# Optimization experiments

Measured on AMD Instinct MI355X. Metric: run time of the kernel, lower is better.

## Reference

```python
import jax, jax.numpy as jnp
import numpy as np

N, E = 50000, 800000
NUM_TYPES = 5
NUM_HEADS = 4
HIDDEN = 32
IN_DIM = 128
NEG_SLOPE = 0.2


def typed_linear(x, types, W):
    # x: [M, in], types: [M] int, W: [T, in, out] -> [M, out]
    out = jnp.zeros((x.shape[0], W.shape[2]), dtype=x.dtype)
    for t in range(W.shape[0]):
        out = out + jnp.where((types == t)[:, None], x @ W[t], jnp.zeros((), x.dtype))
    return out


def setup_inputs() -> dict:
    key = jax.random.key(0)
    ks = jax.random.split(key, 10)
    x = jax.random.normal(ks[0], (N, IN_DIM), dtype=jnp.float32)
    ntype = jax.random.randint(ks[1], (N,), 0, NUM_TYPES)
    etype = jax.random.randint(ks[2], (E,), 0, NUM_TYPES)
    src = jax.random.randint(ks[3], (E,), 0, N)
    dst = jax.random.randint(ks[4], (E,), 0, N)
    sc = 1.0 / np.sqrt(IN_DIM)
    W_typed = jax.random.normal(ks[5], (NUM_TYPES, IN_DIM, HIDDEN * NUM_HEADS), dtype=jnp.float32) * sc
    al_w = jax.random.normal(ks[6], (NUM_TYPES, HIDDEN, HIDDEN), dtype=jnp.float32) * (1.0 / np.sqrt(HIDDEN))
    ar_w = jax.random.normal(ks[7], (NUM_TYPES, HIDDEN, HIDDEN), dtype=jnp.float32) * (1.0 / np.sqrt(HIDDEN))
    W_res = jax.random.normal(ks[8], (IN_DIM, HIDDEN * NUM_HEADS), dtype=jnp.float32) * sc
    b_res = jax.random.normal(ks[9], (HIDDEN * NUM_HEADS,), dtype=jnp.float32) * 0.01
    return {"x": x, "ntype": ntype, "etype": etype, "src": src, "dst": dst,
            "W_typed": W_typed, "al_w": al_w, "ar_w": ar_w, "W_res": W_res, "b_res": b_res}


def reference(x, ntype, etype, src, dst, W_typed, al_w, ar_w, W_res, b_res):
    n = x.shape[0]
    # typed projection W (dropout in the original is applied to `feat` but discarded)
    feat = typed_linear(x, ntype, W_typed)                    # [N, H*D]
    h = feat.reshape(n, NUM_HEADS, HIDDEN)                    # [N, H, D]
    ntype_rep = jnp.repeat(ntype, NUM_HEADS)                  # row n*H+h has node n's type
    h_flat = h.reshape(-1, HIDDEN)
    h_l = typed_linear(h_flat, ntype_rep, al_w).reshape(n, NUM_HEADS, HIDDEN).sum(-1)  # [N, H]
    h_r = typed_linear(h_flat, ntype_rep, ar_w).reshape(n, NUM_HEADS, HIDDEN).sum(-1)  # [N, H]
    e = jax.nn.leaky_relu(h_l[src] + h_r[dst], NEG_SLOPE)     # [E, H]
    # edge softmax grouped by destination node
    m = jax.ops.segment_max(e, dst, num_segments=n)           # [N, H]
    ex = jnp.exp(e - m[dst])
    s = jax.ops.segment_sum(ex, dst, num_segments=n)          # [N, H]
    alpha = ex / s[dst]                                       # [E, H]
    # u_mul_e + sum aggregation
    msg = h[src] * alpha[:, :, None]                          # [E, H, D]
    agg = jax.ops.segment_sum(msg, dst, num_segments=n)       # [N, H, D]
    out = agg.transpose(0, 2, 1).reshape(n, HIDDEN * NUM_HEADS)  # matches permute(0,2,1).view
    out = out + x @ W_res + b_res                             # residual
    return jax.nn.relu(out)                                   # activation
```

## Files before the change

kernel.cpp:

```cpp
#include <hip/hip_runtime.h>
#include <cstdint>
#include <cstddef>

#define IN_DIM 128
#define HID 32
#define NH 4
#define OUT_DIM 128
#define NEG 0.2f
#define NT 5
#define BPT 16
#define NCOLS 272
#define NTILE 17
#define TILE_ELEMS 2048
#define CAPN 50048
#define NE1 144
#define NPREP 40
#define RSHIFT 7
#define SLOT0 16
#define MAXD 56

typedef __attribute__((ext_vector_type(8))) __bf16 bf16x8;
typedef __attribute__((ext_vector_type(4))) float f32x4;

static __device__ __forceinline__ float leaky(float v) { return v > 0.f ? v : NEG * v; }
static __device__ __forceinline__ float blo(unsigned u) { return __uint_as_float(u << 16); }
static __device__ __forceinline__ float bhi(unsigned u) { return __uint_as_float(u & 0xffff0000u); }

static __device__ __forceinline__ void scat1(char* __restrict__ rec, int d, int s) {
    char* rp = rec + ((size_t)d << RSHIFT);
    int r = atomicAdd((int*)rp, 1);
    if (r < MAXD) *(unsigned short*)(rp + SLOT0 + 2 * r) = (unsigned short)s;
}

static __device__ __forceinline__ void scatter4(const int4* __restrict__ dst4,
                                                const int4* __restrict__ src4,
                                                char* __restrict__ rec,
                                                int gid, int E4) {
    if (gid >= E4) return;
    int4 d = dst4[gid];
    int4 s = src4[gid];
    char* rp0 = rec + ((size_t)d.x << RSHIFT);
    char* rp1 = rec + ((size_t)d.y << RSHIFT);
    char* rp2 = rec + ((size_t)d.z << RSHIFT);
    char* rp3 = rec + ((size_t)d.w << RSHIFT);
    int r0 = atomicAdd((int*)rp0, 1);
    int r1 = atomicAdd((int*)rp1, 1);
    int r2 = atomicAdd((int*)rp2, 1);
    int r3 = atomicAdd((int*)rp3, 1);
    if (r0 < MAXD) *(unsigned short*)(rp0 + SLOT0 + 2 * r0) = (unsigned short)s.x;
    if (r1 < MAXD) *(unsigned short*)(rp1 + SLOT0 + 2 * r1) = (unsigned short)s.y;
    if (r2 < MAXD) *(unsigned short*)(rp2 + SLOT0 + 2 * r2) = (unsigned short)s.z;
    if (r3 < MAXD) *(unsigned short*)(rp3 + SLOT0 + 2 * r3) = (unsigned short)s.w;
}

__global__ void __launch_bounds__(256) setup_kernel(
        const int4* __restrict__ dst4, const int4* __restrict__ src4,
        char* __restrict__ rec, int E,
        const int* __restrict__ ntype, int* __restrict__ tcur, int* __restrict__ order,
        int N, int nbs,
        const float* __restrict__ Wt, const float* __restrict__ Wres,
        const float* __restrict__ alw, const float* __restrict__ arw,
        __bf16* __restrict__ Whi, __bf16* __restrict__ Wlo) {
    __shared__ int lc[NT];
    __shared__ int gb[NT];
    __shared__ float alv[HID], arv[HID];
    int bid = blockIdx.x, tid = threadIdx.x;

    if (bid < NE1) {
        int E4 = E >> 2;
        scatter4(dst4, src4, rec, bid * 256 + tid, E4);
        if (bid == 0 && tid == 0) {
            const int* dsts = (const int*)dst4;
            const int* srcs = (const int*)src4;
            for (int e = E4 << 2; e < E; ++e) scat1(rec, dsts[e], srcs[e]);
        }
        return;
    }
    bid -= NE1;
    if (bid < nbs) {
        if (tid < NT) lc[tid] = 0;
        __syncthreads();
        int gid = bid * 256 + tid;
        int t = -1, rank = 0;
        if (gid < N) {
            t = ntype[gid];
            rank = atomicAdd(&lc[t], 1);
        }
        __syncthreads();
        if (tid < NT && lc[tid] > 0) gb[tid] = atomicAdd(&tcur[tid], lc[tid]);
        __syncthreads();
        if (gid < N) order[t * CAPN + gb[t] + rank] = gid;
        return;
    }
    bid -= nbs;
    {
        int t = bid >> 3, part = bid & 7;
        if (tid < 64) {
            int which = tid >= HID;
            int i = tid & (HID - 1);
            const float* p = (which ? arw : alw) + ((size_t)t * HID + i) * HID;
            float s = 0.f;
            for (int j = 0; j < HID; ++j) s += p[j];
            (which ? arv : alv)[i] = s;
        }
        __syncthreads();
        int end = (part + 1) * 4352;
        for (int idx = part * 4352 + tid; idx < end; idx += 256) {
            int n = idx >> 7, k = idx & 127;
            float w;
            if (n < 128) {
                w = Wt[((size_t)t * IN_DIM + k) * OUT_DIM + n];
            } else if (n < 256) {
                w = Wres[(size_t)k * OUT_DIM + (n - 128)];
            } else if (n < 264) {
                int h = (n - 256) & 3;
                const float* av = (n >= 260) ? arv : alv;
                float s = 0.f;
                for (int i = 0; i < HID; ++i)
                    s += Wt[((size_t)t * IN_DIM + k) * OUT_DIM + h * HID + i] * av[i];
                w = s;
            } else {
                w = 0.f;
            }
            __bf16 hi = (__bf16)w;
            __bf16 lo = (__bf16)(w - (float)hi);
            size_t o = (size_t)(t * NTILE + (n >> 4)) * TILE_ELEMS
                     + (size_t)(((k >> 3) * 16 + (n & 15)) << 3) + (k & 7);
            Whi[o] = hi;
            Wlo[o] = lo;
        }
    }
}

__global__ void __launch_bounds__(256) mega2_kernel(
        const int4* __restrict__ dst4, const int4* __restrict__ src4,
        char* __restrict__ rec, int E,
        int e4base, int nbh2,
        const float* __restrict__ x, const int* __restrict__ order,
        const int* __restrict__ tcur,
        const __bf16* __restrict__ Whi, const __bf16* __restrict__ Wlo,
        const float* __restrict__ bres,
        __bf16* __restrict__ h_bf, float* __restrict__ hl, float* __restrict__ hr,
        float* __restrict__ out) {
    __shared__ bf16x8 lds_hi[256];
    __shared__ bf16x8 lds_lo[256];
    __shared__ int nids_s[BPT];
    int bid = blockIdx.x;
    int q = bid / 5, r5 = bid - q * 5;
    int tid = threadIdx.x;

    if (r5 == 4) {
        if (q >= nbh2) return;
        scatter4(dst4, src4, rec, e4base + q * 256 + tid, E >> 2);
        return;
    }

    int b = 4 * q + r5;
    int t = -1, lb = 0, cthis = 0;
    {
        int pbl = 0;
        for (int tt = 0; tt < NT; ++tt) {
            int c = tcur[tt];
            int ntt = (c + BPT - 1) >> 4;
            if (b < pbl + ntt) { t = tt; lb = b - pbl; cthis = c; break; }
            pbl += ntt;
        }
    }
    if (t < 0) return;
    int base = lb * BPT;

    {
        int row = tid >> 4, c = tid & 15;
        int li = base + row;
        int nd = (li < cthis) ? order[t * CAPN + li] : -1;
        if (tid < BPT) nids_s[tid] = (base + tid < cthis) ? order[t * CAPN + base + tid] : -1;
        float4 v0 = make_float4(0.f, 0.f, 0.f, 0.f), v1 = v0;
        if (nd >= 0) {
            const float4* xr = (const float4*)(x + (size_t)nd * IN_DIM + c * 8);
            v0 = xr[0];
            v1 = xr[1];
        }
        float f[8] = {v0.x, v0.y, v0.z, v0.w, v1.x, v1.y, v1.z, v1.w};
        bf16x8 hv, lv;
#pragma unroll
        for (int j = 0; j < 8; ++j) {
            __bf16 h = (__bf16)f[j];
            hv[j] = h;
            lv[j] = (__bf16)(f[j] - (float)h);
        }
        lds_hi[c * 16 + row] = hv;
        lds_lo[c * 16 + row] = lv;
    }
    __syncthreads();

    int w = tid >> 6, lane = tid & 63;
    int lr = lane & 15, lg = lane >> 4;
    bool w3 = (w == 3);

    const __bf16* Wbh = Whi + (size_t)t * NTILE * TILE_ELEMS;
    const __bf16* Wbl = Wlo + (size_t)t * NTILE * TILE_ELEMS;

    f32x4 acc[5];
#pragma unroll
    for (int nt = 0; nt < 5; ++nt) acc[nt] = (f32x4)0.f;

#pragma unroll
    for (int ks = 0; ks < 4; ++ks) {
        int ai = ks * 64 + lg * 16 + lr;
        size_t ao = (size_t)ai << 3;
        bf16x8 ah = lds_hi[ai];
        bf16x8 al = lds_lo[ai];
#pragma unroll
        for (int nt = 0; nt < 5; ++nt) {
            if (nt == 4 && !w3) continue;
            int ng = (nt < 4) ? (nt * 4 + w) : 16;
            bf16x8 bh = *(const bf16x8*)(Wbh + (size_t)ng * TILE_ELEMS + ao);
            acc[nt] = __builtin_amdgcn_mfma_f32_16x16x32_bf16(al, bh, acc[nt], 0, 0, 0);
            acc[nt] = __builtin_amdgcn_mfma_f32_16x16x32_bf16(ah, bh, acc[nt], 0, 0, 0);
            if (nt == 4) {
                bf16x8 bl = *(const bf16x8*)(Wbl + (size_t)16 * TILE_ELEMS + ao);
                acc[4] = __builtin_amdgcn_mfma_f32_16x16x32_bf16(ah, bl, acc[4], 0, 0, 0);
            }
        }
    }

    int nids[4];
#pragma unroll
    for (int r = 0; r < 4; ++r) nids[r] = nids_s[lg * 4 + r];

#pragma unroll
    for (int nt = 0; nt < 5; ++nt) {
        if (nt == 4 && !w3) continue;
        int ng = (nt < 4) ? (nt * 4 + w) : 16;
        int col = ng * 16 + lr;
        float bb = (col >= 128 && col < 256) ? bres[col - 128] : 0.f;
#pragma unroll
        for (int r = 0; r < 4; ++r) {
            int nid = nids[r];
            if (nid < 0) continue;
            float v = acc[nt][r];
            if (col < 128) {
                h_bf[(size_t)nid * OUT_DIM + col] = (__bf16)v;
            } else if (col < 256) {
                out[(size_t)nid * OUT_DIM + (col - 128)] = v + bb;
            } else if (col < 260) {
                hl[nid * NH + (col - 256)] = v;
            } else if (col < 264) {
                hr[nid * NH + (col - 260)] = v;
            }
        }
    }
}

__global__ void agg_kernel(const char* __restrict__ rec,
                           const float* __restrict__ hlf,
                           const float4* __restrict__ hr4, const __bf16* __restrict__ h_bf,
                           float* __restrict__ out, int n_nodes) {
    int gid = blockIdx.x * 256 + threadIdx.x;
    int n = gid >> 4;
    if (n >= n_nodes) return;
    int l = threadIdx.x & 15;
    int myh = l >> 2;
    const char* rp = rec + ((size_t)n << RSHIFT);
    int deg = *(const int*)rp;
    if (deg > MAXD) deg = MAXD;
    const unsigned short* ss = (const unsigned short*)(rp + SLOT0);
    float acc[8];
#pragma unroll
    for (int m = 0; m < 8; ++m) acc[m] = 0.f;

    if (deg > 0) {
        float4 hv = hr4[n];
        float hrh = myh < 2 ? (myh == 0 ? hv.x : hv.y) : (myh == 2 ? hv.z : hv.w);
        float sw = 0.f;
        int k = 0;
        for (; k + 8 <= deg; k += 8) {
            uint4 sp = *(const uint4*)(ss + k);
            int sv[8];
            sv[0] = sp.x & 0xffff; sv[1] = sp.x >> 16;
            sv[2] = sp.y & 0xffff; sv[3] = sp.y >> 16;
            sv[4] = sp.z & 0xffff; sv[5] = sp.z >> 16;
            sv[6] = sp.w & 0xffff; sv[7] = sp.w >> 16;
            uint4 u[8];
            float e[8];
#pragma unroll
            for (int j = 0; j < 8; ++j) {
                u[j] = *(const uint4*)(h_bf + (size_t)sv[j] * OUT_DIM + l * 8);
                e[j] = hlf[sv[j] * 4 + myh];
            }
#pragma unroll
            for (int j = 0; j < 8; ++j) {
                float wv = __expf(leaky(e[j] + hrh));
                sw += wv;
                acc[0] += wv * blo(u[j].x); acc[1] += wv * bhi(u[j].x);
                acc[2] += wv * blo(u[j].y); acc[3] += wv * bhi(u[j].y);
                acc[4] += wv * blo(u[j].z); acc[5] += wv * bhi(u[j].z);
                acc[6] += wv * blo(u[j].w); acc[7] += wv * bhi(u[j].w);
            }
        }
        for (; k < deg; ++k) {
            int sv0 = ss[k];
            uint4 u0 = *(const uint4*)(h_bf + (size_t)sv0 * OUT_DIM + l * 8);
            float e0 = hlf[sv0 * 4 + myh];
            float wv = __expf(leaky(e0 + hrh));
            sw += wv;
            acc[0] += wv * blo(u0.x); acc[1] += wv * bhi(u0.x);
            acc[2] += wv * blo(u0.y); acc[3] += wv * bhi(u0.y);
            acc[4] += wv * blo(u0.z); acc[5] += wv * bhi(u0.z);
            acc[6] += wv * blo(u0.w); acc[7] += wv * bhi(u0.w);
        }
        float inv_s = 1.f / sw;
#pragma unroll
        for (int m = 0; m < 8; ++m) acc[m] *= inv_s;
    }
    size_t ob = (size_t)n * OUT_DIM;
    int based = (l & 3) << 3;
#pragma unroll
    for (int m = 0; m < 8; ++m) {
        int j = ((based + m) << 2) | myh;
        out[ob + j] = fmaxf(acc[m] + out[ob + j], 0.f);
    }
}

extern "C" void kernel_launch(void* const* d_in, const int* in_sizes, int n_in,
                              void* d_out, int out_size, void* d_ws, size_t ws_size,
                              hipStream_t stream) {
    const float* x     = (const float*)d_in[0];
    const int*   ntype = (const int*)d_in[1];
    const int*   src   = (const int*)d_in[3];
    const int*   dst   = (const int*)d_in[4];
    const float* Wt    = (const float*)d_in[5];
    const float* alw   = (const float*)d_in[6];
    const float* arw   = (const float*)d_in[7];
    const float* Wres  = (const float*)d_in[8];
    const float* bres  = (const float*)d_in[9];
    float* out = (float*)d_out;
    int N = in_sizes[1];
    int E = in_sizes[3];

    char* ws = (char*)d_ws;
    size_t off = 0;
    auto alloc = [&](size_t bytes) -> char* {
        char* p = ws + off;
        off += (bytes + 255) & ~(size_t)255;
        return p;
    };
    __bf16* h_bf       = (__bf16*)alloc((size_t)N * OUT_DIM * 2);
    float*  hl         = (float*)alloc((size_t)N * NH * 4);
    float*  hr         = (float*)alloc((size_t)N * NH * 4);
    int*    order      = (int*)alloc((size_t)NT * CAPN * 4);
    __bf16* Whi        = (__bf16*)alloc((size_t)NT * NTILE * TILE_ELEMS * 2);
    __bf16* Wlo        = (__bf16*)alloc((size_t)NT * NTILE * TILE_ELEMS * 2);
    char*   zstart     = ws + off;
    char*   rec        = (char*)alloc((size_t)N << RSHIFT);
    int*    tcur       = (int*)alloc(NT * 4);
    size_t  zlen       = (ws + off) - zstart;

    hipMemsetAsync(zstart, 0, zlen, stream);

    int nbs = (N + 255) / 256;
    int E4 = E >> 2;
    int e4base = NE1 * 256;
    int rem4 = E4 > e4base ? E4 - e4base : 0;
    int nbh2 = (rem4 + 255) / 256;

    setup_kernel<<<NE1 + nbs + NPREP, 256, 0, stream>>>(
        (const int4*)dst, (const int4*)src, rec, E,
        ntype, tcur, order, N, nbs,
        Wt, Wres, alw, arw, Whi, Wlo);

    int pbmax = (N + BPT - 1) / BPT + NT;
    int qproj = (pbmax + 3) / 4;
    int qmax = qproj > nbh2 ? qproj : nbh2;
    mega2_kernel<<<5 * qmax, 256, 0, stream>>>(
        (const int4*)dst, (const int4*)src, rec, E, e4base, nbh2,
        x, order, tcur, Whi, Wlo, bres, h_bf, hl, hr, out);

    agg_kernel<<<(N * 16 + 255) / 256, 256, 0, stream>>>(rec, hl, (const float4*)hr,
                                                         h_bf, out, N);
}
```

Baseline: 117.6 us.

## Replace global atomic edge scatter with two-pass bucketed binning by destination

Edges are first binned into 256-node destination buckets, using a shared-memory histogram and one global atomic per bucket per block. Each bucket is then expanded into per-node adjacency slots inside the projection kernel using only shared-memory atomics. This replaces one global atomic per edge on the padded record array and takes the record array out of the zeroed region, so the memset shrinks. The cost is an extra intermediate buffer pass and a fixed per-bucket capacity (CAPB) that drops edges if a bucket overflows.

```diff
diff --git a/kernel.cpp b/kernel.cpp
--- a/kernel.cpp
+++ b/kernel.cpp
@@ -13,11 +13,12 @@
 #define NTILE 17
 #define TILE_ELEMS 2048
 #define CAPN 50048
-#define NE1 144
 #define NPREP 40
 #define RSHIFT 7
 #define SLOT0 16
 #define MAXD 56
+#define ABLK 2048
+#define CAPB 8192
 
 typedef __attribute__((ext_vector_type(8))) __bf16 bf16x8;
 typedef __attribute__((ext_vector_type(4))) float f32x4;
@@ -26,70 +27,59 @@
 static __device__ __forceinline__ float blo(unsigned u) { return __uint_as_float(u << 16); }
 static __device__ __forceinline__ float bhi(unsigned u) { return __uint_as_float(u & 0xffff0000u); }
 
-static __device__ __forceinline__ void scat1(char* __restrict__ rec, int d, int s) {
-    char* rp = rec + ((size_t)d << RSHIFT);
-    int r = atomicAdd((int*)rp, 1);
-    if (r < MAXD) *(unsigned short*)(rp + SLOT0 + 2 * r) = (unsigned short)s;
-}
-
-static __device__ __forceinline__ void scatter4(const int4* __restrict__ dst4,
-                                                const int4* __restrict__ src4,
-                                                char* __restrict__ rec,
-                                                int gid, int E4) {
-    if (gid >= E4) return;
-    int4 d = dst4[gid];
-    int4 s = src4[gid];
-    char* rp0 = rec + ((size_t)d.x << RSHIFT);
-    char* rp1 = rec + ((size_t)d.y << RSHIFT);
-    char* rp2 = rec + ((size_t)d.z << RSHIFT);
-    char* rp3 = rec + ((size_t)d.w << RSHIFT);
-    int r0 = atomicAdd((int*)rp0, 1);
-    int r1 = atomicAdd((int*)rp1, 1);
-    int r2 = atomicAdd((int*)rp2, 1);
-    int r3 = atomicAdd((int*)rp3, 1);
-    if (r0 < MAXD) *(unsigned short*)(rp0 + SLOT0 + 2 * r0) = (unsigned short)s.x;
-    if (r1 < MAXD) *(unsigned short*)(rp1 + SLOT0 + 2 * r1) = (unsigned short)s.y;
-    if (r2 < MAXD) *(unsigned short*)(rp2 + SLOT0 + 2 * r2) = (unsigned short)s.z;
-    if (r3 < MAXD) *(unsigned short*)(rp3 + SLOT0 + 2 * r3) = (unsigned short)s.w;
-}
-
 __global__ void __launch_bounds__(256) setup_kernel(
-        const int4* __restrict__ dst4, const int4* __restrict__ src4,
-        char* __restrict__ rec, int E,
+        const int* __restrict__ dstp, const int* __restrict__ srcp,
+        unsigned* __restrict__ binned, int* __restrict__ gcur, int E, int nba,
         const int* __restrict__ ntype, int* __restrict__ tcur, int* __restrict__ order,
         int N, int nbs,
         const float* __restrict__ Wt, const float* __restrict__ Wres,
         const float* __restrict__ alw, const float* __restrict__ arw,
         __bf16* __restrict__ Whi, __bf16* __restrict__ Wlo) {
-    __shared__ int lc[NT];
-    __shared__ int gb[NT];
+    __shared__ unsigned pk[ABLK];
+    __shared__ int hist[256], basea[256], cura[256];
     __shared__ float alv[HID], arv[HID];
     int bid = blockIdx.x, tid = threadIdx.x;
 
-    if (bid < NE1) {
-        int E4 = E >> 2;
-        scatter4(dst4, src4, rec, bid * 256 + tid, E4);
-        if (bid == 0 && tid == 0) {
-            const int* dsts = (const int*)dst4;
-            const int* srcs = (const int*)src4;
-            for (int e = E4 << 2; e < E; ++e) scat1(rec, dsts[e], srcs[e]);
+    if (bid < nba) {
+        hist[tid] = 0;
+        cura[tid] = 0;
+        __syncthreads();
+        int e0 = bid * ABLK;
+        int cnt = E - e0;
+        if (cnt > ABLK) cnt = ABLK;
+        for (int k = tid; k < cnt; k += 256) {
+            int d = dstp[e0 + k];
+            int s = srcp[e0 + k];
+            int bb = d >> 8;
+            pk[k] = ((unsigned)bb << 24) | ((unsigned)(d & 255) << 16) | (unsigned)s;
+            atomicAdd(&hist[bb], 1);
+        }
+        __syncthreads();
+        if (hist[tid] > 0) basea[tid] = atomicAdd(&gcur[tid], hist[tid]);
+        __syncthreads();
+        for (int k = tid; k < cnt; k += 256) {
+            unsigned p = pk[k];
+            int bb = p >> 24;
+            int r = atomicAdd(&cura[bb], 1);
+            int pos = basea[bb] + r;
+            if (pos < CAPB) binned[(size_t)bb * CAPB + pos] = p;
         }
         return;
     }
-    bid -= NE1;
+    bid -= nba;
     if (bid < nbs) {
-        if (tid < NT) lc[tid] = 0;
+        if (tid < NT) hist[tid] = 0;
         __syncthreads();
         int gid = bid * 256 + tid;
         int t = -1, rank = 0;
         if (gid < N) {
             t = ntype[gid];
-            rank = atomicAdd(&lc[t], 1);
-        }
-        __syncthreads();
-        if (tid < NT && lc[tid] > 0) gb[tid] = atomicAdd(&tcur[tid], lc[tid]);
-        __syncthreads();
-        if (gid < N) order[t * CAPN + gb[t] + rank] = gid;
+            rank = atomicAdd(&hist[t], 1);
+        }
+        __syncthreads();
+        if (tid < NT && hist[tid] > 0) basea[tid] = atomicAdd(&tcur[tid], hist[tid]);
+        __syncthreads();
+        if (gid < N) order[t * CAPN + basea[t] + rank] = gid;
         return;
     }
     bid -= nbs;
@@ -132,10 +122,9 @@
     }
 }
 
-__global__ void __launch_bounds__(256) mega2_kernel(
-        const int4* __restrict__ dst4, const int4* __restrict__ src4,
-        char* __restrict__ rec, int E,
-        int e4base, int nbh2,
+__global__ void __launch_bounds__(256) mega3_kernel(
+        const unsigned* __restrict__ binned, const int* __restrict__ gcur,
+        char* __restrict__ rec, int N, int nbuck,
         const float* __restrict__ x, const int* __restrict__ order,
         const int* __restrict__ tcur,
         const __bf16* __restrict__ Whi, const __bf16* __restrict__ Wlo,
@@ -145,17 +134,37 @@
     __shared__ bf16x8 lds_hi[256];
     __shared__ bf16x8 lds_lo[256];
     __shared__ int nids_s[BPT];
+    __shared__ int lcnt[256];
     int bid = blockIdx.x;
-    int q = bid / 5, r5 = bid - q * 5;
+    int q = bid / 17, r17 = bid - q * 17;
     int tid = threadIdx.x;
 
-    if (r5 == 4) {
-        if (q >= nbh2) return;
-        scatter4(dst4, src4, rec, e4base + q * 256 + tid, E >> 2);
+    if (r17 == 16) {
+        if (q >= nbuck) return;
+        lcnt[tid] = 0;
+        __syncthreads();
+        int cnt = gcur[q];
+        if (cnt > CAPB) cnt = CAPB;
+        const unsigned* bp = binned + (size_t)q * CAPB;
+        for (int k = tid; k < cnt; k += 256) {
+            unsigned p = bp[k];
+            int dl = (p >> 16) & 255;
+            int r = atomicAdd(&lcnt[dl], 1);
+            if (r < MAXD)
+                *(unsigned short*)(rec + (((size_t)(q << 8) + dl) << RSHIFT) + SLOT0 + 2 * r)
+                    = (unsigned short)(p & 0xffffu);
+        }
+        __syncthreads();
+        int node = (q << 8) + tid;
+        if (node < N) {
+            int c = lcnt[tid];
+            if (c > MAXD) c = MAXD;
+            *(int*)(rec + ((size_t)node << RSHIFT)) = c;
+        }
         return;
     }
 
-    int b = 4 * q + r5;
+    int b = 16 * q + r17;
     int t = -1, lb = 0, cthis = 0;
     {
         int pbl = 0;
@@ -263,7 +272,6 @@
     int myh = l >> 2;
     const char* rp = rec + ((size_t)n << RSHIFT);
     int deg = *(const int*)rp;
-    if (deg > MAXD) deg = MAXD;
     const unsigned short* ss = (const unsigned short*)(rp + SLOT0);
     float acc[8];
 #pragma unroll
@@ -351,29 +359,29 @@
     int*    order      = (int*)alloc((size_t)NT * CAPN * 4);
     __bf16* Whi        = (__bf16*)alloc((size_t)NT * NTILE * TILE_ELEMS * 2);
     __bf16* Wlo        = (__bf16*)alloc((size_t)NT * NTILE * TILE_ELEMS * 2);
+    char*   rec        = (char*)alloc((size_t)N << RSHIFT);
+    unsigned* binned   = (unsigned*)alloc((size_t)256 * CAPB * 4);
     char*   zstart     = ws + off;
-    char*   rec        = (char*)alloc((size_t)N << RSHIFT);
+    int*    gcur       = (int*)alloc(256 * 4);
     int*    tcur       = (int*)alloc(NT * 4);
     size_t  zlen       = (ws + off) - zstart;
 
     hipMemsetAsync(zstart, 0, zlen, stream);
 
     int nbs = (N + 255) / 256;
-    int E4 = E >> 2;
-    int e4base = NE1 * 256;
-    int rem4 = E4 > e4base ? E4 - e4base : 0;
-    int nbh2 = (rem4 + 255) / 256;
-
-    setup_kernel<<<NE1 + nbs + NPREP, 256, 0, stream>>>(
-        (const int4*)dst, (const int4*)src, rec, E,
+    int nba = (E + ABLK - 1) / ABLK;
+    int nbuck = (N + 255) >> 8;
+
+    setup_kernel<<<nba + nbs + NPREP, 256, 0, stream>>>(
+        dst, src, binned, gcur, E, nba,
         ntype, tcur, order, N, nbs,
         Wt, Wres, alw, arw, Whi, Wlo);
 
     int pbmax = (N + BPT - 1) / BPT + NT;
-    int qproj = (pbmax + 3) / 4;
-    int qmax = qproj > nbh2 ? qproj : nbh2;
-    mega2_kernel<<<5 * qmax, 256, 0, stream>>>(
-        (const int4*)dst, (const int4*)src, rec, E, e4base, nbh2,
+    int qproj = (pbmax + 15) / 16;
+    int qmax = qproj > nbuck ? qproj : nbuck;
+    mega3_kernel<<<17 * qmax, 256, 0, stream>>>(
+        binned, gcur, rec, N, nbuck,
         x, order, tcur, Whi, Wlo, bres, h_bf, hl, hr, out);
 
     agg_kernel<<<(N * 16 + 255) / 256, 256, 0, stream>>>(rec, hl, (const float4*)hr,
```

New measurement: 103.5 us. 1.14x faster.
